# Kernel optimization log

Hardware: AMD Instinct MI355X
Metric: run time of the kernel (lower is better)

The kernel has to match this reference:

```python
import jax, jax.numpy as jnp
import numpy as np

N = 50000   # nodes
E = 800000  # edges (avg degree 16)
H = 128     # hidden_dim / emb_dim
OUT = 128   # out_dim
NUM_BOND_TYPE = 6
NUM_BOND_DIR = 6


def setup_inputs() -> dict:
    key = jax.random.key(0)
    ks = jax.random.split(key, 12)
    s = 0.05
    return {
        "x": jax.random.normal(ks[0], (N, H), jnp.float32),
        "edge_index": jax.random.randint(ks[1], (2, E), 0, N),
        "edge_attr": jax.random.randint(ks[2], (E, 2), 0, 6),
        "prelu_a": jnp.float32(0.25),  # PReLU single shared slope (torch default)
        "W_enc": jax.random.normal(ks[3], (H, H), jnp.float32) * s,  # enc_to_dec, no bias
        "edge_emb1": jax.random.normal(ks[4], (NUM_BOND_TYPE, H), jnp.float32) * s,
        "edge_emb2": jax.random.normal(ks[5], (NUM_BOND_DIR, H), jnp.float32) * s,
        "W1": jax.random.normal(ks[6], (H, 2 * H), jnp.float32) * s,
        "b1": jnp.zeros((2 * H,), jnp.float32),
        "W2": jax.random.normal(ks[7], (2 * H, OUT), jnp.float32) * s,
        "b2": jnp.zeros((OUT,), jnp.float32),
    }


def reference(x, edge_index, edge_attr, prelu_a, W_enc, edge_emb1, edge_emb2, W1, b1, W2, b2):
    n = x.shape[0]
    # GNNDecoder: PReLU then enc_to_dec linear (no bias)
    x = jnp.where(x > 0, x, prelu_a * x)
    x = x @ W_enc

    # GINConv.forward: add self loops, self-loop edge_attr = [5, 0]
    loop = jnp.arange(n)
    src = jnp.concatenate([edge_index[0], loop])  # [E+N]
    dst = jnp.concatenate([edge_index[1], loop])  # [E+N]
    ea1 = jnp.concatenate([edge_attr[:, 0], jnp.full((n,), 5, edge_attr.dtype)])
    ea2 = jnp.concatenate([edge_attr[:, 1], jnp.zeros((n,), edge_attr.dtype)])

    # edge embedding lookup + gather-add message + scatter-add aggregate
    edge_emb = edge_emb1[ea1] + edge_emb2[ea2]          # [E+N, H]
    msg = x[src] + edge_emb                             # message(x_j, edge_attr)
    agg = jax.ops.segment_sum(msg, dst, num_segments=n)  # aggr='add'

    # update: MLP Linear(H,2H) -> SiLU -> Linear(2H,OUT)
    h = jax.nn.silu(agg @ W1 + b1)
    return h @ W2 + b2
```

## Files before the change

kernel.cpp:

```cpp
#include <hip/hip_runtime.h>

typedef unsigned short u16;
typedef unsigned int   u32;
typedef __attribute__((ext_vector_type(8))) short short8;
typedef __attribute__((ext_vector_type(4))) float f32x4;

__device__ __forceinline__ float bl(u32 u){ union{u32 i; float f;} c; c.i = u << 16; return c.f; }
__device__ __forceinline__ float bh(u32 u){ union{u32 i; float f;} c; c.i = u & 0xffff0000u; return c.f; }
__device__ __forceinline__ u16 f2b(float f){
  union{float f; u32 i;} c; c.f = f;
  return (u16)((c.i + 0x8000u) >> 16);
}
__device__ __forceinline__ u32 pk2(float a, float b){
  union{float f; u32 i;} x, y; x.f = a; y.f = b;
  return ((x.i + 0x8000u) >> 16) | ((y.i + 0x8000u) & 0xffff0000u);
}

__device__ __forceinline__ void wave_scan_bsum(
    const int* __restrict__ bsum, int nb, int* __restrict__ sPre, int t)
{
  int carry = 0;
  for (int c0 = 0; c0 < nb; c0 += 64) {
    int idx = c0 + t;
    int b = (idx < nb) ? bsum[idx] : 0;
    int v = b;
    #pragma unroll
    for (int d = 1; d < 64; d <<= 1) {
      int u = __shfl_up(v, d);
      if (t >= d) v += u;
    }
    if (idx < nb) sPre[idx] = carry + v - b;
    carry += __shfl(v, 63);
  }
}

__global__ __launch_bounds__(256) void k_setup(
    const float* __restrict__ Wenc, const float* __restrict__ W1,
    const float* __restrict__ W2, const float* __restrict__ e1,
    const float* __restrict__ e2, u16* __restrict__ WencT,
    u16* __restrict__ W1T, u16* __restrict__ W2T,
    float* __restrict__ embF, int* __restrict__ cnt, int N)
{
  int i = blockIdx.x * 256 + threadIdx.x;
  if (i < 16384) {
    int n = i >> 7, k = i & 127;
    WencT[i] = f2b(Wenc[k * 128 + n]);
  } else if (i < 49152) {
    int j = i - 16384;
    int n = j >> 7, k = j & 127;
    W1T[j] = f2b(W1[k * 256 + n]);
  } else if (i < 81920) {
    int j = i - 49152;
    int n = j >> 8, k = j & 255;
    W2T[j] = f2b(W2[k * 128 + n]);
  } else if (i < 81920 + 4608) {
    int j = i - 81920;
    int comb = j >> 7, k = j & 127;
    int c1 = comb / 6, c2 = comb - c1 * 6;
    embF[j] = e1[c1 * 128 + k] + e2[c2 * 128 + k];
  } else {
    int j = i - 81920 - 4608;
    if (j < N) cnt[j] = 0;
  }
}

__global__ __launch_bounds__(256) void k_enc_count(
    const float* __restrict__ x, const float* __restrict__ pa,
    const u16* __restrict__ WT, u16* __restrict__ xencQ, int N,
    const int* __restrict__ ei, int* __restrict__ cnt,
    int* __restrict__ rank, int E, int encBlocks)
{
  if ((int)blockIdx.x >= encBlocks) {
    int e = ((int)blockIdx.x - encBlocks) * 256 + threadIdx.x;
    if (e < E) rank[e] = atomicAdd(&cnt[ei[E + e]], 1);
    return;
  }

  const int K = 128, SK = 136, NT = 8;
  __shared__ u16 sB[128 * SK];

  const int t = threadIdx.x;
  #pragma unroll
  for (int j = 0; j < 8; j++) {
    int i = t + 256 * j;
    int n = i >> 4, k8 = i & 15;
    *(uint4*)&sB[n * SK + k8 * 8] = *(const uint4*)&WT[n * K + k8 * 8];
  }
  __syncthreads();

  const float slope = pa[0];
  const int lane = t & 63, wave = t >> 6, quad = lane >> 4, l16 = lane & 15;
  const int m0 = blockIdx.x * 128 + wave * 32;
  if (m0 >= N) return;

  f32x4 acc[2][NT];
  #pragma unroll
  for (int mr = 0; mr < 2; mr++)
    #pragma unroll
    for (int nt = 0; nt < NT; nt++) acc[mr][nt] = (f32x4){0.f, 0.f, 0.f, 0.f};

  #pragma unroll
  for (int ks = 0; ks < 4; ks++) {
    const int k0 = ks * 32 + quad * 8;
    union { u32 u[4]; short8 s; } a[2];
    #pragma unroll
    for (int mr = 0; mr < 2; mr++) {
      int row = m0 + mr * 16 + l16; row = min(row, N - 1);
      const float4* ap = (const float4*)&x[(size_t)row * 128 + k0];
      float4 f0 = ap[0], f1 = ap[1];
      float v0 = f0.x > 0.f ? f0.x : slope * f0.x;
      float v1 = f0.y > 0.f ? f0.y : slope * f0.y;
      float v2 = f0.z > 0.f ? f0.z : slope * f0.z;
      float v3 = f0.w > 0.f ? f0.w : slope * f0.w;
      float v4 = f1.x > 0.f ? f1.x : slope * f1.x;
      float v5 = f1.y > 0.f ? f1.y : slope * f1.y;
      float v6 = f1.z > 0.f ? f1.z : slope * f1.z;
      float v7 = f1.w > 0.f ? f1.w : slope * f1.w;
      a[mr].u[0] = pk2(v0, v1); a[mr].u[1] = pk2(v2, v3);
      a[mr].u[2] = pk2(v4, v5); a[mr].u[3] = pk2(v6, v7);
    }
    #pragma unroll
    for (int nt = 0; nt < NT; nt++) {
      short8 b = *(const short8*)&sB[(nt * 16 + l16) * SK + k0];
      acc[0][nt] = __builtin_amdgcn_mfma_f32_16x16x32_bf16(a[0].s, b, acc[0][nt], 0, 0, 0);
      acc[1][nt] = __builtin_amdgcn_mfma_f32_16x16x32_bf16(a[1].s, b, acc[1][nt], 0, 0, 0);
    }
  }

  #pragma unroll
  for (int mr = 0; mr < 2; mr++)
    #pragma unroll
    for (int nt = 0; nt < NT; nt++) {
      int col = nt * 16 + l16;
      int q = col >> 5, cq = col & 31;
      #pragma unroll
      for (int r = 0; r < 4; r++) {
        int row = m0 + mr * 16 + quad * 4 + r;
        if (row < N)
          xencQ[((size_t)q * N + row) * 32 + cq] = f2b(acc[mr][nt][r]);
      }
    }
}

__global__ __launch_bounds__(256) void k_scan_block(
    const int* __restrict__ cnt, int* __restrict__ offs,
    int* __restrict__ bsum, int n)
{
  __shared__ int sS[256];
  const int b = blockIdx.x, t = threadIdx.x;
  const int i0 = b * 1024 + t * 4;
  int4 v = make_int4(0, 0, 0, 0);
  if (i0 + 3 < n) v = *(const int4*)&cnt[i0];
  else {
    if (i0     < n) v.x = cnt[i0];
    if (i0 + 1 < n) v.y = cnt[i0 + 1];
    if (i0 + 2 < n) v.z = cnt[i0 + 2];
  }
  int s = v.x + v.y + v.z + v.w;
  sS[t] = s;
  __syncthreads();
  for (int d = 1; d < 256; d <<= 1) {
    int val = (t >= d) ? sS[t - d] : 0;
    __syncthreads();
    sS[t] += val;
    __syncthreads();
  }
  int ex = sS[t] - s;
  if (t == 255) bsum[b] = sS[t];
  int o0 = ex, o1 = o0 + v.x, o2 = o1 + v.y, o3 = o2 + v.z;
  if (i0     < n) offs[i0]     = o0;
  if (i0 + 1 < n) offs[i0 + 1] = o1;
  if (i0 + 2 < n) offs[i0 + 2] = o2;
  if (i0 + 3 < n) offs[i0 + 3] = o3;
}

__global__ __launch_bounds__(256) void k_fill(
    const int* __restrict__ ei, const int* __restrict__ ea,
    const int* __restrict__ offs, const int* __restrict__ rank,
    const int* __restrict__ bsum, int nb,
    u32* __restrict__ recs, int E)
{
  __shared__ int sPre[256];
  const int t = threadIdx.x;
  if (t < 64) wave_scan_bsum(bsum, nb, sPre, t);
  __syncthreads();

  int e = blockIdx.x * 256 + t;
  if (e >= E) return;
  int src = ei[e];
  int dst = ei[E + e];
  int2 a = *(const int2*)&ea[2 * e];
  int pos = offs[dst] + sPre[dst >> 10] + rank[e];
  recs[pos] = (u32)src | ((u32)(a.x * 6 + a.y) << 26);
}

__global__ __launch_bounds__(256) void k_gather(
    const int* __restrict__ offs, const int* __restrict__ bsum, int nb,
    const u32* __restrict__ recs, const float* __restrict__ embF,
    const u32* __restrict__ xencQ, u32* __restrict__ aggbQ, int N, int E)
{
  const int ES = 36;
  __shared__ float sE4[4 * 36 * ES];
  __shared__ int sPre[256];

  const int t = threadIdx.x;
  for (int i = t; i < 4 * 36 * 8; i += 256) {
    int q = i / (36 * 8);
    int r = i - q * 36 * 8;
    int c = r >> 3, s4 = r & 7;
    float4 v = *(const float4*)&embF[c * 128 + q * 32 + s4 * 4];
    *(float4*)&sE4[(q * 36 + c) * ES + s4 * 4] = v;
  }
  if (t < 64) wave_scan_bsum(bsum, nb, sPre, t);
  __syncthreads();

  const int lane = t & 63, wave = t >> 6;
  const int g = lane >> 3, sub = lane & 7;
  const int v = blockIdx.x * 32 + wave * 8 + g;
  const bool vok = v < N;
  const int vc = vok ? v : N - 1;
  const int beg = offs[vc] + sPre[vc >> 10];
  const int end = (vc == N - 1) ? E : (offs[vc + 1] + sPre[(vc + 1) >> 10]);
  const int deg = vok ? end - beg : 0;
  const u32 M = 0x3ffffffu;

  #pragma unroll
  for (int q = 0; q < 4; q++) {
    const u32* xq = xencQ + (size_t)q * N * 16;
    const float* sEq = &sE4[q * 36 * ES];

    uint2 xs = *(const uint2*)&xq[(size_t)vc * 16 + sub * 2];
    float4 es = *(const float4*)&sEq[30 * ES + sub * 4];
    float a0 = bl(xs.x) + es.x, a1 = bh(xs.x) + es.y;
    float a2 = bl(xs.y) + es.z, a3 = bh(xs.y) + es.w;

    for (int j0 = 0; j0 < deg; j0 += 8) {
      int idx = beg + j0 + sub;
      u32 rv = recs[min(idx, end - 1)];
      #pragma unroll
      for (int k = 0; k < 8; k++) {
        u32 r = __shfl(rv, (lane & 56) + k);
        if (j0 + k < deg) {
          uint2 xr = *(const uint2*)&xq[(size_t)(r & M) * 16 + sub * 2];
          float4 er = *(const float4*)&sEq[(r >> 26) * ES + sub * 4];
          a0 += bl(xr.x) + er.x;  a1 += bh(xr.x) + er.y;
          a2 += bl(xr.y) + er.z;  a3 += bh(xr.y) + er.w;
        }
      }
    }

    if (vok) {
      uint2 o;
      o.x = pk2(a0, a1);
      o.y = pk2(a2, a3);
      *(uint2*)&aggbQ[((size_t)q * N + vc) * 16 + sub * 2] = o;
    }
  }
}

__global__ __launch_bounds__(256) void k_mlp(
    const u16* __restrict__ aggbQ, const u16* __restrict__ W1T,
    const float* __restrict__ b1, const u16* __restrict__ W2T,
    const float* __restrict__ b2, float* __restrict__ out, int N)
{
  const int SK = 136;
  __shared__ u16 sW[128 * SK];
  __shared__ u16 sH[128 * SK];
  __shared__ float sB1[256];
  __shared__ float sB2[128];

  const int t = threadIdx.x;
  const int lane = t & 63, wave = t >> 6, quad = lane >> 4, l16 = lane & 15;
  const int m0 = blockIdx.x * 128 + wave * 32;

  if (t < 128) sB2[t] = b2[t];
  sB1[t] = b1[t];

  union { uint4 q; short8 s; } a[2][4];
  #pragma unroll
  for (int mr = 0; mr < 2; mr++) {
    int row = min(m0 + mr * 16 + l16, N - 1);
    #pragma unroll
    for (int ks = 0; ks < 4; ks++)
      a[mr][ks].q = *(const uint4*)&aggbQ[((size_t)ks * N + row) * 32 + quad * 8];
  }

  f32x4 acc2[2][8];
  #pragma unroll
  for (int mr = 0; mr < 2; mr++)
    #pragma unroll
    for (int nt = 0; nt < 8; nt++) acc2[mr][nt] = (f32x4){0.f, 0.f, 0.f, 0.f};

  for (int half = 0; half < 2; half++) {
    #pragma unroll
    for (int j = 0; j < 8; j++) {
      int i = t + 256 * j;
      int n = i >> 4, k8 = i & 15;
      *(uint4*)&sW[n * SK + k8 * 8] =
          *(const uint4*)&W1T[(size_t)(half * 128 + n) * 128 + k8 * 8];
    }
    __syncthreads();

    f32x4 acc1[2][8];
    #pragma unroll
    for (int mr = 0; mr < 2; mr++)
      #pragma unroll
      for (int nt = 0; nt < 8; nt++) acc1[mr][nt] = (f32x4){0.f, 0.f, 0.f, 0.f};

    #pragma unroll
    for (int ks = 0; ks < 4; ks++) {
      const int k0 = ks * 32 + quad * 8;
      #pragma unroll
      for (int nt = 0; nt < 8; nt++) {
        short8 b = *(const short8*)&sW[(nt * 16 + l16) * SK + k0];
        acc1[0][nt] = __builtin_amdgcn_mfma_f32_16x16x32_bf16(a[0][ks].s, b, acc1[0][nt], 0, 0, 0);
        acc1[1][nt] = __builtin_amdgcn_mfma_f32_16x16x32_bf16(a[1][ks].s, b, acc1[1][nt], 0, 0, 0);
      }
    }

    #pragma unroll
    for (int mr = 0; mr < 2; mr++)
      #pragma unroll
      for (int nt = 0; nt < 8; nt++) {
        int col = nt * 16 + l16;
        float bias = sB1[half * 128 + col];
        #pragma unroll
        for (int r = 0; r < 4; r++) {
          float z = acc1[mr][nt][r] + bias;
          float s = z / (1.f + __expf(-z));
          sH[(wave * 32 + mr * 16 + quad * 4 + r) * SK + col] = f2b(s);
        }
      }
    __syncthreads();

    #pragma unroll
    for (int j = 0; j < 8; j++) {
      int i = t + 256 * j;
      int n = i >> 4, k8 = i & 15;
      *(uint4*)&sW[n * SK + k8 * 8] =
          *(const uint4*)&W2T[(size_t)n * 256 + half * 128 + k8 * 8];
    }
    __syncthreads();

    #pragma unroll
    for (int ks = 0; ks < 4; ks++) {
      const int k0 = ks * 32 + quad * 8;
      union { uint4 q; short8 s; } ah[2];
      #pragma unroll
      for (int mr = 0; mr < 2; mr++)
        ah[mr].q = *(const uint4*)&sH[(wave * 32 + mr * 16 + l16) * SK + k0];
      #pragma unroll
      for (int nt = 0; nt < 8; nt++) {
        short8 b = *(const short8*)&sW[(nt * 16 + l16) * SK + k0];
        acc2[0][nt] = __builtin_amdgcn_mfma_f32_16x16x32_bf16(ah[0].s, b, acc2[0][nt], 0, 0, 0);
        acc2[1][nt] = __builtin_amdgcn_mfma_f32_16x16x32_bf16(ah[1].s, b, acc2[1][nt], 0, 0, 0);
      }
    }
    __syncthreads();
  }

  #pragma unroll
  for (int mr = 0; mr < 2; mr++)
    #pragma unroll
    for (int nt = 0; nt < 8; nt++) {
      int col = nt * 16 + l16;
      float bias = sB2[col];
      #pragma unroll
      for (int r = 0; r < 4; r++) {
        int row = m0 + mr * 16 + quad * 4 + r;
        if (row < N) out[(size_t)row * 128 + col] = acc2[mr][nt][r] + bias;
      }
    }
}

extern "C" void kernel_launch(void* const* d_in, const int* in_sizes, int n_in,
                              void* d_out, int out_size, void* d_ws, size_t ws_size,
                              hipStream_t stream) {
  const float* x    = (const float*)d_in[0];
  const int*   ei   = (const int*)d_in[1];
  const int*   ea   = (const int*)d_in[2];
  const float* pa   = (const float*)d_in[3];
  const float* Wenc = (const float*)d_in[4];
  const float* e1   = (const float*)d_in[5];
  const float* e2   = (const float*)d_in[6];
  const float* W1   = (const float*)d_in[7];
  const float* b1   = (const float*)d_in[8];
  const float* W2   = (const float*)d_in[9];
  const float* b2   = (const float*)d_in[10];
  float* out = (float*)d_out;

  const int N = in_sizes[0] / 128;
  const int E = in_sizes[1] / 2;

  char* ws = (char*)d_ws;
  size_t off = 0;
  auto alloc = [&](size_t bytes) {
    void* p = ws + off;
    off = (off + bytes + 255) & ~(size_t)255;
    return p;
  };
  u16*   xencQ  = (u16*)  alloc((size_t)N * 128 * 2);
  u32*   aggbQ  = (u32*)  alloc((size_t)N * 64 * 4);
  int*   cnt    = (int*)  alloc((size_t)N * 4);
  int*   offs   = (int*)  alloc((size_t)(N + 1) * 4);
  int*   rank   = (int*)  alloc((size_t)E * 4);
  int*   bsum   = (int*)  alloc(256 * 4);
  u32*   recs   = (u32*)  alloc((size_t)E * 4);
  u16*   WencT  = (u16*)  alloc(128 * 128 * 2);
  u16*   W1T    = (u16*)  alloc(256 * 128 * 2);
  u16*   W2T    = (u16*)  alloc(128 * 256 * 2);
  float* embF   = (float*)alloc(36 * 128 * 4);

  const int encBlocks   = (N + 127) / 128;
  const int edgeBlocks  = (E + 255) / 256;
  const int setupBlocks = (81920 + 4608 + N + 255) / 256;
  const int nb          = (N + 1023) / 1024;
  const int gatherBlocks = (N + 31) / 32;

  k_setup<<<setupBlocks, 256, 0, stream>>>(Wenc, W1, W2, e1, e2,
                                           WencT, W1T, W2T, embF, cnt, N);
  k_enc_count<<<encBlocks + edgeBlocks, 256, 0, stream>>>(
      x, pa, WencT, xencQ, N, ei, cnt, rank, E, encBlocks);
  k_scan_block<<<nb, 256, 0, stream>>>(cnt, offs, bsum, N);
  k_fill<<<edgeBlocks, 256, 0, stream>>>(ei, ea, offs, rank, bsum, nb, recs, E);
  k_gather<<<gatherBlocks, 256, 0, stream>>>(
      offs, bsum, nb, recs, embF, (const u32*)xencQ, aggbQ, N, E);
  k_mlp<<<encBlocks, 256, 0, stream>>>(
      (const u16*)aggbQ, W1T, b1, W2T, b2, out, N);
}
```

Before: 233.0 us.

## Prefetch edge records and double-buffer gathers; fold setup into other kernels

The gather kernel now loads the first 32 edge records up front and issues two batches of 8 neighbor-row loads before accumulating them, so more loads are in flight at once. It also keeps the edge embeddings in shared memory as packed bf16 instead of fp32. The separate setup kernel is removed: the Wenc transpose moves into the encoder blocks, the W1/W2/embedding prep is appended as extra blocks to the scan kernel, and cnt is zeroed with a memset, which saves one launch. The costs are more registers in the gather (capped with launch bounds of 256,4) and redundant per-block Wenc conversion with scalar strided shared-memory stores.

```diff
diff --git a/kernel.cpp b/kernel.cpp
--- a/kernel.cpp
+++ b/kernel.cpp
@@ -34,39 +34,9 @@
   }
 }
 
-__global__ __launch_bounds__(256) void k_setup(
-    const float* __restrict__ Wenc, const float* __restrict__ W1,
-    const float* __restrict__ W2, const float* __restrict__ e1,
-    const float* __restrict__ e2, u16* __restrict__ WencT,
-    u16* __restrict__ W1T, u16* __restrict__ W2T,
-    float* __restrict__ embF, int* __restrict__ cnt, int N)
-{
-  int i = blockIdx.x * 256 + threadIdx.x;
-  if (i < 16384) {
-    int n = i >> 7, k = i & 127;
-    WencT[i] = f2b(Wenc[k * 128 + n]);
-  } else if (i < 49152) {
-    int j = i - 16384;
-    int n = j >> 7, k = j & 127;
-    W1T[j] = f2b(W1[k * 256 + n]);
-  } else if (i < 81920) {
-    int j = i - 49152;
-    int n = j >> 8, k = j & 255;
-    W2T[j] = f2b(W2[k * 128 + n]);
-  } else if (i < 81920 + 4608) {
-    int j = i - 81920;
-    int comb = j >> 7, k = j & 127;
-    int c1 = comb / 6, c2 = comb - c1 * 6;
-    embF[j] = e1[c1 * 128 + k] + e2[c2 * 128 + k];
-  } else {
-    int j = i - 81920 - 4608;
-    if (j < N) cnt[j] = 0;
-  }
-}
-
 __global__ __launch_bounds__(256) void k_enc_count(
     const float* __restrict__ x, const float* __restrict__ pa,
-    const u16* __restrict__ WT, u16* __restrict__ xencQ, int N,
+    const float* __restrict__ Wenc, u16* __restrict__ xencQ, int N,
     const int* __restrict__ ei, int* __restrict__ cnt,
     int* __restrict__ rank, int E, int encBlocks)
 {
@@ -76,15 +46,14 @@
     return;
   }
 
-  const int K = 128, SK = 136, NT = 8;
+  const int SK = 136, NT = 8;
   __shared__ u16 sB[128 * SK];
 
   const int t = threadIdx.x;
-  #pragma unroll
-  for (int j = 0; j < 8; j++) {
+  for (int j = 0; j < 64; j++) {
     int i = t + 256 * j;
-    int n = i >> 4, k8 = i & 15;
-    *(uint4*)&sB[n * SK + k8 * 8] = *(const uint4*)&WT[n * K + k8 * 8];
+    int k = i >> 7, n = i & 127;
+    sB[n * SK + k] = f2b(Wenc[i]);
   }
   __syncthreads();
 
@@ -142,10 +111,34 @@
     }
 }
 
-__global__ __launch_bounds__(256) void k_scan_block(
+__global__ __launch_bounds__(256) void k_scanW(
     const int* __restrict__ cnt, int* __restrict__ offs,
-    int* __restrict__ bsum, int n)
-{
+    int* __restrict__ bsum, int n, int nb,
+    const float* __restrict__ W1, const float* __restrict__ W2,
+    const float* __restrict__ e1, const float* __restrict__ e2,
+    u16* __restrict__ W1T, u16* __restrict__ W2T, u32* __restrict__ embP)
+{
+  if ((int)blockIdx.x >= nb) {
+    int i = ((int)blockIdx.x - nb) * 256 + threadIdx.x;
+    if (i < 32768) {
+      int nn = i >> 7, k = i & 127;
+      W1T[i] = f2b(W1[k * 256 + nn]);
+    } else if (i < 65536) {
+      int j = i - 32768;
+      int nn = j >> 8, k = j & 255;
+      W2T[j] = f2b(W2[k * 128 + nn]);
+    } else {
+      int j = i - 65536;
+      int q = j / 576, rem = j - q * 576;
+      int c = rem >> 4, s = rem & 15;
+      int c1 = c / 6, c2 = c - c1 * 6;
+      int col = q * 32 + s * 2;
+      embP[j] = pk2(e1[c1 * 128 + col]     + e2[c2 * 128 + col],
+                    e1[c1 * 128 + col + 1] + e2[c2 * 128 + col + 1]);
+    }
+    return;
+  }
+
   __shared__ int sS[256];
   const int b = blockIdx.x, t = threadIdx.x;
   const int i0 = b * 1024 + t * 4;
@@ -194,65 +187,102 @@
   recs[pos] = (u32)src | ((u32)(a.x * 6 + a.y) << 26);
 }
 
-__global__ __launch_bounds__(256) void k_gather(
+struct B8 { uint2 x[8]; u32 r[8]; };
+
+__device__ __forceinline__ void issue8(B8& b, u32 rv, int grp,
+                                       const u32* __restrict__ xq, int sub) {
+  #pragma unroll
+  for (int k = 0; k < 8; k++) {
+    u32 r = __shfl(rv, grp + k);
+    b.r[k] = r;
+    b.x[k] = *(const uint2*)&xq[(size_t)(r & 0x3ffffffu) * 16 + sub * 2];
+  }
+}
+
+__device__ __forceinline__ void acc8(float* a, const B8& b,
+                                     const u32* __restrict__ sEq,
+                                     int sub, int dleft) {
+  #pragma unroll
+  for (int k = 0; k < 8; k++) {
+    if (k < dleft) {
+      uint2 e = *(const uint2*)&sEq[(b.r[k] >> 26) * 18 + sub * 2];
+      uint2 x = b.x[k];
+      a[0] += bl(x.x) + bl(e.x);  a[1] += bh(x.x) + bh(e.x);
+      a[2] += bl(x.y) + bl(e.y);  a[3] += bh(x.y) + bh(e.y);
+    }
+  }
+}
+
+__global__ __launch_bounds__(256, 4) void k_gather(
     const int* __restrict__ offs, const int* __restrict__ bsum, int nb,
-    const u32* __restrict__ recs, const float* __restrict__ embF,
+    const u32* __restrict__ recs, const u32* __restrict__ embP,
     const u32* __restrict__ xencQ, u32* __restrict__ aggbQ, int N, int E)
 {
-  const int ES = 36;
-  __shared__ float sE4[4 * 36 * ES];
+  const int ES = 18;
+  __shared__ u32 sE[4 * 36 * ES];
   __shared__ int sPre[256];
 
   const int t = threadIdx.x;
-  for (int i = t; i < 4 * 36 * 8; i += 256) {
-    int q = i / (36 * 8);
-    int r = i - q * 36 * 8;
-    int c = r >> 3, s4 = r & 7;
-    float4 v = *(const float4*)&embF[c * 128 + q * 32 + s4 * 4];
-    *(float4*)&sE4[(q * 36 + c) * ES + s4 * 4] = v;
+  for (int i = t; i < 4 * 36 * 16; i += 256) {
+    int qc = i >> 4, s = i & 15;
+    sE[qc * ES + s] = embP[i];
   }
   if (t < 64) wave_scan_bsum(bsum, nb, sPre, t);
   __syncthreads();
 
   const int lane = t & 63, wave = t >> 6;
-  const int g = lane >> 3, sub = lane & 7;
-  const int v = blockIdx.x * 32 + wave * 8 + g;
+  const int grp = lane & 56, sub = lane & 7;
+  const int v = blockIdx.x * 32 + wave * 8 + (lane >> 3);
   const bool vok = v < N;
   const int vc = vok ? v : N - 1;
   const int beg = offs[vc] + sPre[vc >> 10];
   const int end = (vc == N - 1) ? E : (offs[vc + 1] + sPre[(vc + 1) >> 10]);
-  const int deg = vok ? end - beg : 0;
-  const u32 M = 0x3ffffffu;
-
-  #pragma unroll
+  const int d = vok ? end - beg : 0;
+
+  u32 rv0 = 0, rv1 = 0, rv2 = 0, rv3 = 0;
+  if (d > 0)  rv0 = recs[min(beg + sub, end - 1)];
+  if (d > 8)  rv1 = recs[min(beg + 8 + sub, end - 1)];
+  if (d > 16) rv2 = recs[min(beg + 16 + sub, end - 1)];
+  if (d > 24) rv3 = recs[min(beg + 24 + sub, end - 1)];
+
+  #pragma unroll 1
   for (int q = 0; q < 4; q++) {
     const u32* xq = xencQ + (size_t)q * N * 16;
-    const float* sEq = &sE4[q * 36 * ES];
+    const u32* sEq = &sE[q * 36 * ES];
 
     uint2 xs = *(const uint2*)&xq[(size_t)vc * 16 + sub * 2];
-    float4 es = *(const float4*)&sEq[30 * ES + sub * 4];
-    float a0 = bl(xs.x) + es.x, a1 = bh(xs.x) + es.y;
-    float a2 = bl(xs.y) + es.z, a3 = bh(xs.y) + es.w;
-
-    for (int j0 = 0; j0 < deg; j0 += 8) {
-      int idx = beg + j0 + sub;
-      u32 rv = recs[min(idx, end - 1)];
-      #pragma unroll
-      for (int k = 0; k < 8; k++) {
-        u32 r = __shfl(rv, (lane & 56) + k);
-        if (j0 + k < deg) {
-          uint2 xr = *(const uint2*)&xq[(size_t)(r & M) * 16 + sub * 2];
-          float4 er = *(const float4*)&sEq[(r >> 26) * ES + sub * 4];
-          a0 += bl(xr.x) + er.x;  a1 += bh(xr.x) + er.y;
-          a2 += bl(xr.y) + er.z;  a3 += bh(xr.y) + er.w;
+    uint2 es = *(const uint2*)&sEq[30 * ES + sub * 2];
+    float a[4];
+    a[0] = bl(xs.x) + bl(es.x);  a[1] = bh(xs.x) + bh(es.x);
+    a[2] = bl(xs.y) + bl(es.y);  a[3] = bh(xs.y) + bh(es.y);
+
+    if (d > 0) {
+      B8 bA, bB;
+      issue8(bA, rv0, grp, xq, sub);
+      if (d > 8) issue8(bB, rv1, grp, xq, sub);
+      acc8(a, bA, sEq, sub, d);
+      if (d > 8) {
+        if (d > 16) issue8(bA, rv2, grp, xq, sub);
+        acc8(a, bB, sEq, sub, d - 8);
+        if (d > 16) {
+          if (d > 24) issue8(bB, rv3, grp, xq, sub);
+          acc8(a, bA, sEq, sub, d - 16);
+          if (d > 24) {
+            acc8(a, bB, sEq, sub, d - 24);
+            for (int j0 = 32; j0 < d; j0 += 8) {
+              u32 rvt = recs[min(beg + j0 + sub, end - 1)];
+              issue8(bA, rvt, grp, xq, sub);
+              acc8(a, bA, sEq, sub, d - j0);
+            }
+          }
         }
       }
     }
 
     if (vok) {
       uint2 o;
-      o.x = pk2(a0, a1);
-      o.y = pk2(a2, a3);
+      o.x = pk2(a[0], a[1]);
+      o.y = pk2(a[2], a[3]);
       *(uint2*)&aggbQ[((size_t)q * N + vc) * 16 + sub * 2] = o;
     }
   }
@@ -405,26 +435,24 @@
   int*   offs   = (int*)  alloc((size_t)(N + 1) * 4);
   int*   rank   = (int*)  alloc((size_t)E * 4);
   int*   bsum   = (int*)  alloc(256 * 4);
-  u32*   recs   = (u32*)  alloc((size_t)E * 4);
-  u16*   WencT  = (u16*)  alloc(128 * 128 * 2);
+  u32*   recs   = (u32*)  alloc((size_t)(E + 64) * 4);
   u16*   W1T    = (u16*)  alloc(256 * 128 * 2);
   u16*   W2T    = (u16*)  alloc(128 * 256 * 2);
-  float* embF   = (float*)alloc(36 * 128 * 4);
-
-  const int encBlocks   = (N + 127) / 128;
-  const int edgeBlocks  = (E + 255) / 256;
-  const int setupBlocks = (81920 + 4608 + N + 255) / 256;
-  const int nb          = (N + 1023) / 1024;
+  u32*   embP   = (u32*)  alloc(2304 * 4);
+
+  const int encBlocks    = (N + 127) / 128;
+  const int edgeBlocks   = (E + 255) / 256;
+  const int nb           = (N + 1023) / 1024;
   const int gatherBlocks = (N + 31) / 32;
 
-  k_setup<<<setupBlocks, 256, 0, stream>>>(Wenc, W1, W2, e1, e2,
-                                           WencT, W1T, W2T, embF, cnt, N);
+  hipMemsetAsync(cnt, 0, (size_t)N * 4, stream);
   k_enc_count<<<encBlocks + edgeBlocks, 256, 0, stream>>>(
-      x, pa, WencT, xencQ, N, ei, cnt, rank, E, encBlocks);
-  k_scan_block<<<nb, 256, 0, stream>>>(cnt, offs, bsum, N);
+      x, pa, Wenc, xencQ, N, ei, cnt, rank, E, encBlocks);
+  k_scanW<<<nb + 265, 256, 0, stream>>>(
+      cnt, offs, bsum, N, nb, W1, W2, e1, e2, W1T, W2T, embP);
   k_fill<<<edgeBlocks, 256, 0, stream>>>(ei, ea, offs, rank, bsum, nb, recs, E);
   k_gather<<<gatherBlocks, 256, 0, stream>>>(
-      offs, bsum, nb, recs, embF, (const u32*)xencQ, aggbQ, N, E);
+      offs, bsum, nb, recs, embP, (const u32*)xencQ, aggbQ, N, E);
   k_mlp<<<encBlocks, 256, 0, stream>>>(
       (const u16*)aggbQ, W1T, b1, W2T, b2, out, N);
 }
```

New measurement: 224.0 us. -3.9%, faster.
